# Kernel tuning notes

Measured on AMD Instinct MI355X. Metric: run time of the kernel, lower is better.

The kernel has to match this reference:

```python
import jax, jax.numpy as jnp
import numpy as np

VOCAB = 32000
D_MODEL = 768
D_STATE = 16
D_CONV = 4
EXPAND = 2
D_INNER = EXPAND * D_MODEL          # 1536
DT_RANK = (D_MODEL + 15) // 16      # 48
B, L = 2, 1024


def setup_inputs() -> dict:
    key = jax.random.key(0)
    ks = jax.random.split(key, 10)
    s = 0.02
    return {
        "input_ids": jax.random.randint(ks[0], (B, L), 0, VOCAB),
        "embedding": jax.random.normal(ks[1], (VOCAB, D_MODEL), jnp.float32) * s,
        "in_proj_w": jax.random.normal(ks[2], (D_MODEL, 2 * D_INNER), jnp.float32) * s,
        "conv_w": jax.random.normal(ks[3], (D_INNER, D_CONV), jnp.float32) * s,
        "conv_b": jnp.zeros((D_INNER,), jnp.float32),
        "x_proj_w": jax.random.normal(ks[4], (D_INNER, DT_RANK + 2 * D_STATE), jnp.float32) * s,
        "dt_proj_w": jax.random.normal(ks[5], (DT_RANK, D_INNER), jnp.float32) * s,
        "dt_proj_b": jax.random.normal(ks[6], (D_INNER,), jnp.float32) * 0.1,
        "A_log": jnp.log(jnp.broadcast_to(
            jnp.arange(1, D_STATE + 1, dtype=jnp.float32), (D_INNER, D_STATE))),
        "D": jnp.ones((D_INNER,), jnp.float32),
        "out_proj_w": jax.random.normal(ks[7], (D_INNER, D_MODEL), jnp.float32) * s,
        "lm_head_w": jax.random.normal(ks[8], (D_MODEL, VOCAB), jnp.float32) * s,
        "lm_head_b": jnp.zeros((VOCAB,), jnp.float32),
    }


def _mamba(x, in_proj_w, conv_w, conv_b, x_proj_w, dt_proj_w, dt_proj_b,
           A_log, D, out_proj_w):
    Bsz = x.shape[0]
    # input projection -> (x, z) gate branches, each [B,L,D_INNER]
    xz = x @ in_proj_w
    xi, z = jnp.split(xz, 2, axis=-1)
    # causal depthwise conv1d over time
    xc = jax.lax.conv_general_dilated(
        xi.transpose(0, 2, 1), conv_w[:, None, :],
        window_strides=(1,), padding=[(D_CONV - 1, 0)],
        feature_group_count=D_INNER,
        dimension_numbers=("NCH", "OIH", "NCH"))
    xa = jax.nn.silu(xc + conv_b[None, :, None]).transpose(0, 2, 1)  # [B,L,Din]
    # input-dependent SSM params
    dbl = xa @ x_proj_w                                   # [B,L,dt_rank+2N]
    dt = dbl[..., :DT_RANK]
    Bm = dbl[..., DT_RANK:DT_RANK + D_STATE]              # [B,L,N]
    Cm = dbl[..., DT_RANK + D_STATE:]                     # [B,L,N]
    dt = jax.nn.softplus(dt @ dt_proj_w + dt_proj_b)      # [B,L,Din]
    A = -jnp.exp(A_log)                                   # [Din,N]
    dA = jnp.exp(dt[..., None] * A)                       # [B,L,Din,N]
    dBu = dt[..., None] * Bm[:, :, None, :] * xa[..., None]

    def step(h, ins):
        dA_t, dBu_t, C_t = ins
        h = dA_t * h + dBu_t                              # [B,Din,N]
        return h, jnp.einsum("bdn,bn->bd", h, C_t)

    h0 = jnp.zeros((Bsz, D_INNER, D_STATE), x.dtype)
    _, ys = jax.lax.scan(
        step, h0,
        (dA.transpose(1, 0, 2, 3), dBu.transpose(1, 0, 2, 3),
         Cm.transpose(1, 0, 2)))
    y = ys.transpose(1, 0, 2) + xa * D                    # skip connection
    y = y * jax.nn.silu(z)                                # gate
    return y @ out_proj_w


def reference(input_ids, embedding, in_proj_w, conv_w, conv_b, x_proj_w,
              dt_proj_w, dt_proj_b, A_log, D, out_proj_w, lm_head_w, lm_head_b):
    x = embedding[input_ids]                              # [B,L,d_model]
    y = _mamba(x, in_proj_w, conv_w, conv_b, x_proj_w, dt_proj_w, dt_proj_b,
               A_log, D, out_proj_w)
    return y @ lm_head_w + lm_head_b                      # [B,L,vocab]
```

## Files before the change

kernel.cpp:

```cpp
#include <hip/hip_runtime.h>
#include <hip/hip_bf16.h>
#include <cstdio>
#include <cstdint>

#define B_SZ    2
#define L_SEQ   1024
#define DMODEL  768
#define DINNER  1536
#define DSTATE  16
#define DTRANK  48
#define VOCAB   32000
#define BL      (B_SZ * L_SEQ)
#define NCH     64
#define CLEN    16

typedef __bf16 bf16;
typedef __bf16 bf16x8 __attribute__((ext_vector_type(8)));
typedef __bf16 bf16x4 __attribute__((ext_vector_type(4)));
typedef float  f32x4  __attribute__((ext_vector_type(4)));

__device__ __forceinline__ void gload16(const void* g, void* l) {
  __builtin_amdgcn_global_load_lds(
      (const __attribute__((address_space(1))) void*)g,
      (__attribute__((address_space(3))) void*)l, 16, 0, 0);
}
__device__ __forceinline__ void memfence() { asm volatile("" ::: "memory"); }

__global__ void k_embed(const int* __restrict__ ids, const float* __restrict__ emb,
                        bf16* __restrict__ xh, bf16* __restrict__ xl) {
  const int row = blockIdx.x;
  const int id  = ids[row];
  const float4* s = (const float4*)(emb + (size_t)id * DMODEL);
  const int i = threadIdx.x;
  const float4 v = s[i];
  bf16x4 hv, lv;
  hv[0] = (bf16)v.x; hv[1] = (bf16)v.y; hv[2] = (bf16)v.z; hv[3] = (bf16)v.w;
  lv[0] = (bf16)(v.x - (float)hv[0]); lv[1] = (bf16)(v.y - (float)hv[1]);
  lv[2] = (bf16)(v.z - (float)hv[2]); lv[3] = (bf16)(v.w - (float)hv[3]);
  *(bf16x4*)(xh + (size_t)row * DMODEL + i * 4) = hv;
  *(bf16x4*)(xl + (size_t)row * DMODEL + i * 4) = lv;
}

template<bool SPLIT>
__global__ void k_tconv(const float* __restrict__ W, bf16* __restrict__ Th,
                        bf16* __restrict__ Tl, int K, int N) {
  __shared__ float t[32][33];
  const int n0 = blockIdx.x * 32;
  const int k0 = blockIdx.y * 32;
  const int tx = threadIdx.x;
  const int ty = threadIdx.y;
#pragma unroll
  for (int i = 0; i < 4; i++)
    t[ty + i * 8][tx] = W[(size_t)(k0 + ty + i * 8) * N + n0 + tx];
  __syncthreads();
#pragma unroll
  for (int i = 0; i < 4; i++) {
    const float v = t[tx][ty + i * 8];
    const bf16 hv = (bf16)v;
    Th[(size_t)(n0 + ty + i * 8) * K + k0 + tx] = hv;
    if constexpr (SPLIT)
      Tl[(size_t)(n0 + ty + i * 8) * K + k0 + tx] = (bf16)(v - (float)hv);
  }
}

template<bool SPLIT, bool BIAS, bool BF16OUT>
__global__ __launch_bounds__(256) void k_gemm(
    const bf16* __restrict__ Ah, const bf16* __restrict__ Al,
    const bf16* __restrict__ Bh, const bf16* __restrict__ Bl,
    const float* __restrict__ bias, float* __restrict__ C,
    int M, int N, int K) {
  __shared__ bf16 sAh[2][128 * 32];
  __shared__ bf16 sBh[2][128 * 32];
  __shared__ bf16 sAl[SPLIT ? 2 : 1][SPLIT ? 128 * 32 : 8];
  __shared__ bf16 sBl[SPLIT ? 2 : 1][SPLIT ? 128 * 32 : 8];

  const int tid  = threadIdx.x;
  const int lane = tid & 63;
  const int wave = tid >> 6;
  const int bm = blockIdx.y * 128;
  const int bn = blockIdx.x * 128;

  const int srow = tid >> 2;
  const int schk = (tid & 3) * 8;

  const bf16* gA0 = Ah + (size_t)(bm + srow) * K + schk;
  const bf16* gA1 = gA0 + (size_t)64 * K;
  const bf16* gB0 = Bh + (size_t)(bn + srow) * K + schk;
  const bf16* gB1 = gB0 + (size_t)64 * K;
  const bf16 *gA0l = nullptr, *gA1l = nullptr, *gB0l = nullptr, *gB1l = nullptr;
  if constexpr (SPLIT) {
    gA0l = Al + (size_t)(bm + srow) * K + schk;  gA1l = gA0l + (size_t)64 * K;
    gB0l = Bl + (size_t)(bn + srow) * K + schk;  gB1l = gB0l + (size_t)64 * K;
  }

  const int wm = (wave >> 1) * 64;
  const int wn = (wave & 1) * 64;
  const int lr = lane & 15;
  const int kg = lane >> 4;

  f32x4 acc[4][4] = {};
  const int nt = K >> 5;

#define STG(t_, b_) do {                                                    \
    const size_t ko_ = (size_t)(t_) * 32;                                   \
    gload16(gA0 + ko_, &sAh[b_][tid * 8]);                                  \
    gload16(gA1 + ko_, &sAh[b_][2048 + tid * 8]);                           \
    gload16(gB0 + ko_, &sBh[b_][tid * 8]);                                  \
    gload16(gB1 + ko_, &sBh[b_][2048 + tid * 8]);                           \
    if constexpr (SPLIT) {                                                  \
      gload16(gA0l + ko_, &sAl[b_][tid * 8]);                               \
      gload16(gA1l + ko_, &sAl[b_][2048 + tid * 8]);                        \
      gload16(gB0l + ko_, &sBl[b_][tid * 8]);                               \
      gload16(gB1l + ko_, &sBl[b_][2048 + tid * 8]);                        \
    }                                                                       \
  } while (0)

  STG(0, 0);
  asm volatile("s_waitcnt vmcnt(0)" ::: "memory");
  __builtin_amdgcn_s_barrier();
  memfence();

  for (int t = 0; t < nt; ++t) {
    const int b = t & 1;
    if (t + 1 < nt) STG(t + 1, b ^ 1);

    bf16x8 af[4], bfv[4];
#pragma unroll
    for (int i = 0; i < 4; i++)
      af[i] = *(const bf16x8*)&sAh[b][(wm + i * 16 + lr) * 32 + kg * 8];
#pragma unroll
    for (int i = 0; i < 4; i++)
      bfv[i] = *(const bf16x8*)&sBh[b][(wn + i * 16 + lr) * 32 + kg * 8];

#pragma unroll
    for (int mi = 0; mi < 4; mi++)
#pragma unroll
      for (int ni = 0; ni < 4; ni++)
        acc[mi][ni] = __builtin_amdgcn_mfma_f32_16x16x32_bf16(
            af[mi], bfv[ni], acc[mi][ni], 0, 0, 0);

    if constexpr (SPLIT) {
      bf16x8 afl[4], bfl[4];
#pragma unroll
      for (int i = 0; i < 4; i++)
        afl[i] = *(const bf16x8*)&sAl[b][(wm + i * 16 + lr) * 32 + kg * 8];
#pragma unroll
      for (int i = 0; i < 4; i++)
        bfl[i] = *(const bf16x8*)&sBl[b][(wn + i * 16 + lr) * 32 + kg * 8];
#pragma unroll
      for (int mi = 0; mi < 4; mi++)
#pragma unroll
        for (int ni = 0; ni < 4; ni++) {
          acc[mi][ni] = __builtin_amdgcn_mfma_f32_16x16x32_bf16(
              afl[mi], bfv[ni], acc[mi][ni], 0, 0, 0);
          acc[mi][ni] = __builtin_amdgcn_mfma_f32_16x16x32_bf16(
              af[mi], bfl[ni], acc[mi][ni], 0, 0, 0);
        }
    }

    asm volatile("s_waitcnt vmcnt(0)" ::: "memory");
    __builtin_amdgcn_s_barrier();
    memfence();
  }
#undef STG

#pragma unroll
  for (int mi = 0; mi < 4; mi++) {
#pragma unroll
    for (int ni = 0; ni < 4; ni++) {
      const int col = bn + wn + ni * 16 + lr;
      float bv = 0.f;
      if constexpr (BIAS) bv = bias[col];
#pragma unroll
      for (int r = 0; r < 4; r++) {
        const int row = bm + wm + mi * 16 + kg * 4 + r;
        if constexpr (BF16OUT)
          ((bf16*)C)[(size_t)row * N + col] = (bf16)(acc[mi][ni][r] + bv);
        else
          C[(size_t)row * N + col] = acc[mi][ni][r] + bv;
      }
    }
  }
}

__global__ __launch_bounds__(512, 4) void k_gemm8(
    const bf16* __restrict__ A, const bf16* __restrict__ Bt,
    const float* __restrict__ bias, float* __restrict__ C,
    int M, int N, int K, int mblocks) {
  extern __shared__ bf16 lds[];

  const int orig = (blockIdx.x & 7) * ((int)gridDim.x >> 3) + (blockIdx.x >> 3);
  const int bm = (orig % mblocks) * 128;
  const int bn = (orig / mblocks) * 256;

  const int tid  = threadIdx.x;
  const int lane = tid & 63;
  const int wave = tid >> 6;
  const int wm   = wave >> 2;
  const int wn   = wave & 3;
  const int lr   = lane & 15;
  const int kg   = lane >> 4;
  const int sw   = (lr >> 1) & 3;

  const int srA = (wave << 4) + (lane >> 2);
  const int srB = (wave << 5) + (lane >> 2);
  const int ssA = (lane & 3) ^ ((srA >> 1) & 3);
  const int ssB = (lane & 3) ^ ((srB >> 1) & 3);
  const size_t gAoff  = (size_t)(bm + srA) * K + ssA * 8;
  const size_t gBoff0 = (size_t)(bn + srB) * K + ssB * 8;
  const size_t gBoff1 = gBoff0 + (size_t)16 * K;

  const int aoff = (wm * 64 + lr) * 32 + ((kg ^ sw) << 3);
  const int boff = (wn * 64 + lr) * 32 + ((kg ^ sw) << 3);

  const int nt = K >> 5;

#define STAGE(ts_) do {                                                    \
    bf16* lb_ = lds + ((ts_) & 1) * 12288;                                 \
    const size_t ko_ = (size_t)(ts_) * 32;                                 \
    gload16(A  + gAoff  + ko_, lb_ + wave * 512);                          \
    gload16(Bt + gBoff0 + ko_, lb_ + 4096 + wave * 1024);                  \
    gload16(Bt + gBoff1 + ko_, lb_ + 4096 + wave * 1024 + 512);            \
  } while (0)

  f32x4 acc[4][4] = {};

  STAGE(0);
  asm volatile("s_waitcnt vmcnt(0)" ::: "memory");
  __builtin_amdgcn_s_barrier();
  memfence();

  for (int t = 0; t < nt; ++t) {
    if (t + 1 < nt) STAGE(t + 1);

    const bf16* lA = lds + (t & 1) * 12288;
    const bf16* lB = lA + 4096;

    bf16x8 bfr[4], afr[4];
#pragma unroll
    for (int j = 0; j < 4; j++) bfr[j] = *(const bf16x8*)(lB + boff + j * 512);
#pragma unroll
    for (int i = 0; i < 4; i++) afr[i] = *(const bf16x8*)(lA + aoff + i * 512);

    __builtin_amdgcn_s_setprio(1);
#pragma unroll
    for (int i = 0; i < 4; i++)
#pragma unroll
      for (int j = 0; j < 4; j++)
        acc[i][j] = __builtin_amdgcn_mfma_f32_16x16x32_bf16(afr[i], bfr[j], acc[i][j], 0, 0, 0);
    __builtin_amdgcn_s_setprio(0);

    asm volatile("s_waitcnt vmcnt(0)" ::: "memory");
    __builtin_amdgcn_s_barrier();
    memfence();
  }
#undef STAGE

  float bv[4];
#pragma unroll
  for (int j = 0; j < 4; j++)
    bv[j] = bias ? bias[bn + wn * 64 + j * 16 + lr] : 0.f;
#pragma unroll
  for (int i = 0; i < 4; i++) {
    const int row = bm + wm * 64 + i * 16 + kg * 4;
#pragma unroll
    for (int j = 0; j < 4; j++) {
      const int col = bn + wn * 64 + j * 16 + lr;
#pragma unroll
      for (int r = 0; r < 4; r++)
        C[(size_t)(row + r) * N + col] = acc[i][j][r] + bv[j];
    }
  }
}

__global__ void k_conv(const float* __restrict__ xz, const float* __restrict__ cw,
                       const float* __restrict__ cb, float* __restrict__ xa) {
  const int bl = blockIdx.x;
  const int l  = bl & (L_SEQ - 1);
  for (int d = threadIdx.x; d < DINNER; d += blockDim.x) {
    float acc = cb[d];
#pragma unroll
    for (int k = 0; k < 4; k++) {
      const int ll = l + k - 3;
      if (ll >= 0)
        acc = fmaf(xz[(size_t)(bl + k - 3) * (2 * DINNER) + d], cw[d * 4 + k], acc);
    }
    xa[(size_t)bl * DINNER + d] = acc / (1.f + __expf(-acc));
  }
}

__global__ void k_xproj(const float* __restrict__ xa, const float* __restrict__ w,
                        float* __restrict__ dbl) {
  const int t = threadIdx.x;
  const int r = blockIdx.x * 8 + t / 80;
  const int c = t % 80;
  const float* xr = xa + (size_t)r * DINNER;
  float acc = 0.f;
  for (int k = 0; k < DINNER; k++) acc = fmaf(xr[k], w[k * 80 + c], acc);
  dbl[(size_t)r * 80 + c] = acc;
}

__global__ __launch_bounds__(256) void k_dtproj(
    const float* __restrict__ dbl, const float* __restrict__ w,
    const float* __restrict__ bvec, float* __restrict__ dt) {
  const int r0 = blockIdx.x * 8;
  const int tid = threadIdx.x;
  __shared__ float ds[8][DTRANK];
  for (int i = tid; i < 8 * DTRANK; i += 256)
    ds[i / DTRANK][i % DTRANK] = dbl[(size_t)(r0 + i / DTRANK) * 80 + i % DTRANK];
  __syncthreads();
  for (int c = tid; c < DINNER; c += 256) {
    const float bvc = bvec[c];
    float acc[8];
#pragma unroll
    for (int j = 0; j < 8; j++) acc[j] = bvc;
    for (int k = 0; k < DTRANK; k++) {
      const float wv = w[(size_t)k * DINNER + c];
#pragma unroll
      for (int j = 0; j < 8; j++) acc[j] = fmaf(ds[j][k], wv, acc[j]);
    }
#pragma unroll
    for (int j = 0; j < 8; j++) {
      const float a = acc[j];
      dt[(size_t)(r0 + j) * DINNER + c] = (a > 20.f) ? a : log1pf(expf(a));
    }
  }
}

__global__ __launch_bounds__(256) void k_scan1(
    const float* __restrict__ dt, const float* __restrict__ dbl,
    const float* __restrict__ xa, const float* __restrict__ a_log,
    float* __restrict__ P, float* __restrict__ S) {
  const int tid = threadIdx.x;
  const int d = blockIdx.x * 256 + tid;
  const int c = blockIdx.y;
  const int b = blockIdx.z;
  __shared__ float sB[CLEN][DSTATE];
  {
    const int j = tid >> 4, n = tid & 15;
    sB[j][n] = dbl[(size_t)(b * L_SEQ + c * CLEN + j) * 80 + DTRANK + n];
  }
  __syncthreads();
  float a[16];
#pragma unroll
  for (int q = 0; q < 4; q++) {
    const float4 v = *(const float4*)&a_log[d * DSTATE + q * 4];
    a[q*4+0] = -expf(v.x); a[q*4+1] = -expf(v.y);
    a[q*4+2] = -expf(v.z); a[q*4+3] = -expf(v.w);
  }
  float h[16] = {}, p[16];
#pragma unroll
  for (int n = 0; n < 16; n++) p[n] = 1.f;
  const size_t rowb = (size_t)(b * L_SEQ + c * CLEN);
#pragma unroll 4
  for (int j = 0; j < CLEN; j++) {
    const size_t row = rowb + j;
    const float dtv = dt[row * DINNER + d];
    const float xav = xa[row * DINNER + d];
    const float du  = dtv * xav;
#pragma unroll
    for (int n = 0; n < 16; n++) {
      const float dA = __expf(dtv * a[n]);
      h[n] = fmaf(dA, h[n], du * sB[j][n]);
      p[n] *= dA;
    }
  }
  const size_t base = (((size_t)c * B_SZ + b) * DINNER + d) * DSTATE;
#pragma unroll
  for (int q = 0; q < 4; q++) {
    *(float4*)&P[base + q * 4] = make_float4(p[q*4], p[q*4+1], p[q*4+2], p[q*4+3]);
    *(float4*)&S[base + q * 4] = make_float4(h[q*4], h[q*4+1], h[q*4+2], h[q*4+3]);
  }
}

__global__ __launch_bounds__(256) void k_scan2(
    const float* __restrict__ P, const float* __restrict__ S,
    float* __restrict__ Hin) {
  const int gid = blockIdx.x * 256 + threadIdx.x;
  const int STRIDE = B_SZ * DINNER * DSTATE;
  float h = 0.f;
#pragma unroll 4
  for (int c = 0; c < NCH; c++) {
    Hin[(size_t)c * STRIDE + gid] = h;
    h = fmaf(P[(size_t)c * STRIDE + gid], h, S[(size_t)c * STRIDE + gid]);
  }
}

__global__ __launch_bounds__(256) void k_scan3(
    const float* __restrict__ dt, const float* __restrict__ dbl,
    const float* __restrict__ xa, const float* __restrict__ a_log,
    const float* __restrict__ dvec, const float* __restrict__ xz,
    const float* __restrict__ Hin, bf16* __restrict__ ych,
    bf16* __restrict__ ycl) {
  const int tid = threadIdx.x;
  const int d = blockIdx.x * 256 + tid;
  const int c = blockIdx.y;
  const int b = blockIdx.z;
  __shared__ float sB[CLEN][DSTATE];
  __shared__ float sC[CLEN][DSTATE];
  {
    const int j = tid >> 4, n = tid & 15;
    const size_t r80 = (size_t)(b * L_SEQ + c * CLEN + j) * 80;
    sB[j][n] = dbl[r80 + DTRANK + n];
    sC[j][n] = dbl[r80 + DTRANK + DSTATE + n];
  }
  __syncthreads();
  float a[16];
#pragma unroll
  for (int q = 0; q < 4; q++) {
    const float4 v = *(const float4*)&a_log[d * DSTATE + q * 4];
    a[q*4+0] = -expf(v.x); a[q*4+1] = -expf(v.y);
    a[q*4+2] = -expf(v.z); a[q*4+3] = -expf(v.w);
  }
  float h[16];
  const size_t base = (((size_t)c * B_SZ + b) * DINNER + d) * DSTATE;
#pragma unroll
  for (int q = 0; q < 4; q++) {
    const float4 v = *(const float4*)&Hin[base + q * 4];
    h[q*4+0] = v.x; h[q*4+1] = v.y; h[q*4+2] = v.z; h[q*4+3] = v.w;
  }
  const float Dv = dvec[d];
  const size_t rowb = (size_t)(b * L_SEQ + c * CLEN);
#pragma unroll 4
  for (int j = 0; j < CLEN; j++) {
    const size_t row = rowb + j;
    const float dtv = dt[row * DINNER + d];
    const float xav = xa[row * DINNER + d];
    const float du  = dtv * xav;
    float y = 0.f;
#pragma unroll
    for (int n = 0; n < 16; n++) {
      const float dA = __expf(dtv * a[n]);
      h[n] = fmaf(dA, h[n], du * sB[j][n]);
      y = fmaf(h[n], sC[j][n], y);
    }
    const float z  = xz[row * (2 * DINNER) + DINNER + d];
    const float sz = z / (1.f + __expf(-z));
    const float val = fmaf(xav, Dv, y) * sz;
    const bf16 hv = (bf16)val;
    ych[row * DINNER + d] = hv;
    ycl[row * DINNER + d] = (bf16)(val - (float)hv);
  }
}

extern "C" void kernel_launch(void* const* d_in, const int* in_sizes, int n_in,
                              void* d_out, int out_size, void* d_ws, size_t ws_size,
                              hipStream_t stream) {
  const int*   ids   = (const int*)d_in[0];
  const float* emb   = (const float*)d_in[1];
  const float* w_in  = (const float*)d_in[2];
  const float* cw    = (const float*)d_in[3];
  const float* cb    = (const float*)d_in[4];
  const float* w_x   = (const float*)d_in[5];
  const float* w_dt  = (const float*)d_in[6];
  const float* b_dt  = (const float*)d_in[7];
  const float* a_log = (const float*)d_in[8];
  const float* dvec  = (const float*)d_in[9];
  const float* w_out = (const float*)d_in[10];
  const float* w_lm  = (const float*)d_in[11];
  const float* b_lm  = (const float*)d_in[12];
  float* out = (float*)d_out;

  char* ws = (char*)d_ws;
  size_t off = 0;
  auto alloc = [&](size_t bytes) {
    void* p = ws + off;
    off = (off + bytes + 255) & ~(size_t)255;
    return p;
  };
  float* xw    = (float*)alloc((size_t)BL * DMODEL * 4);
  float* xz    = (float*)alloc((size_t)BL * 2 * DINNER * 4);
  float* xa    = (float*)alloc((size_t)BL * DINNER * 4);
  float* dbl   = (float*)alloc((size_t)BL * 80 * 4);
  float* dt    = (float*)alloc((size_t)BL * DINNER * 4);
  float* ycmb  = (float*)alloc((size_t)BL * DINNER * 4);
  float* yo    = (float*)alloc((size_t)BL * DMODEL * 4);
  bf16* xwh    = (bf16*)alloc((size_t)BL * DMODEL * 2);
  bf16* xwl    = (bf16*)alloc((size_t)BL * DMODEL * 2);
  bf16* wtinh  = (bf16*)alloc((size_t)3072 * DMODEL * 2);
  bf16* wtinl  = (bf16*)alloc((size_t)3072 * DMODEL * 2);
  bf16* ych    = (bf16*)alloc((size_t)BL * DINNER * 2);
  bf16* ycl    = (bf16*)alloc((size_t)BL * DINNER * 2);
  bf16* wtoh   = (bf16*)alloc((size_t)DMODEL * DINNER * 2);
  bf16* wtol   = (bf16*)alloc((size_t)DMODEL * DINNER * 2);
  bf16* yob    = (bf16*)alloc((size_t)BL * DMODEL * 2);
  bf16* wtlm   = (bf16*)alloc((size_t)VOCAB * DMODEL * 2);
  (void)xw; (void)ycmb; (void)yo;
  if (off > ws_size) {
    fprintf(stderr, "kernel_launch: ws too small (need %zu, have %zu)\n", off, ws_size);
    return;
  }

  float* Pbuf = (float*)xwh;
  float* Sbuf = (float*)ych;
  float* Hin  = (float*)wtlm;

  (void)hipFuncSetAttribute((const void*)k_gemm8,
                            hipFuncAttributeMaxDynamicSharedMemorySize, 65536);

  k_embed<<<BL, DMODEL / 4, 0, stream>>>(ids, emb, xwh, xwl);
  k_tconv<true><<<dim3(3072 / 32, DMODEL / 32), dim3(32, 8), 0, stream>>>(w_in, wtinh, wtinl, DMODEL, 3072);
  k_gemm<true, false, false><<<dim3(3072 / 128, BL / 128), 256, 0, stream>>>(
      xwh, xwl, wtinh, wtinl, nullptr, xz, BL, 3072, DMODEL);
  k_conv<<<BL, 256, 0, stream>>>(xz, cw, cb, xa);
  k_xproj<<<BL / 8, 640, 0, stream>>>(xa, w_x, dbl);
  k_dtproj<<<BL / 8, 256, 0, stream>>>(dbl, w_dt, b_dt, dt);
  k_scan1<<<dim3(DINNER / 256, NCH, B_SZ), 256, 0, stream>>>(dt, dbl, xa, a_log, Pbuf, Sbuf);
  k_scan2<<<(B_SZ * DINNER * DSTATE) / 256, 256, 0, stream>>>(Pbuf, Sbuf, Hin);
  k_scan3<<<dim3(DINNER / 256, NCH, B_SZ), 256, 0, stream>>>(dt, dbl, xa, a_log, dvec, xz, Hin, ych, ycl);
  k_tconv<true><<<dim3(DMODEL / 32, DINNER / 32), dim3(32, 8), 0, stream>>>(w_out, wtoh, wtol, DINNER, DMODEL);
  k_gemm<true, false, true><<<dim3(DMODEL / 128, BL / 128), 256, 0, stream>>>(
      ych, ycl, wtoh, wtol, nullptr, (float*)yob, BL, DMODEL, DINNER);
  k_tconv<false><<<dim3(VOCAB / 32, DMODEL / 32), dim3(32, 8), 0, stream>>>(w_lm, wtlm, nullptr, DMODEL, VOCAB);
  {
    const int mb = BL / 128;
    const int nb = VOCAB / 256;
    k_gemm8<<<mb * nb, 512, 49152, stream>>>(yob, wtlm, b_lm, out,
                                             BL, VOCAB, DMODEL, mb);
  }
}
```

Before: 467.4 us.

## Load GEMM A operand directly from global into registers, bypass LDS

Both GEMM kernels stop staging the A tile through shared memory. Each wave now loads its A fragments straight from global memory into registers at the top of every k-step, and only B stays double-buffered in LDS. The lm_head GEMM's dynamic LDS allocation shrinks to match, and B staging is re-indexed. This cuts LDS traffic and footprint, which may raise occupancy. The cost is that A global loads are issued per wave with no prefetch, so their latency sits directly before the MFMAs. A is also re-read by waves sharing the same rows, relying on cache.

```diff
diff --git a/kernel.cpp b/kernel.cpp
--- a/kernel.cpp
+++ b/kernel.cpp
@@ -69,9 +69,7 @@
     const bf16* __restrict__ Bh, const bf16* __restrict__ Bl,
     const float* __restrict__ bias, float* __restrict__ C,
     int M, int N, int K) {
-  __shared__ bf16 sAh[2][128 * 32];
   __shared__ bf16 sBh[2][128 * 32];
-  __shared__ bf16 sAl[SPLIT ? 2 : 1][SPLIT ? 128 * 32 : 8];
   __shared__ bf16 sBl[SPLIT ? 2 : 1][SPLIT ? 128 * 32 : 8];
 
   const int tid  = threadIdx.x;
@@ -83,13 +81,10 @@
   const int srow = tid >> 2;
   const int schk = (tid & 3) * 8;
 
-  const bf16* gA0 = Ah + (size_t)(bm + srow) * K + schk;
-  const bf16* gA1 = gA0 + (size_t)64 * K;
   const bf16* gB0 = Bh + (size_t)(bn + srow) * K + schk;
   const bf16* gB1 = gB0 + (size_t)64 * K;
-  const bf16 *gA0l = nullptr, *gA1l = nullptr, *gB0l = nullptr, *gB1l = nullptr;
+  const bf16 *gB0l = nullptr, *gB1l = nullptr;
   if constexpr (SPLIT) {
-    gA0l = Al + (size_t)(bm + srow) * K + schk;  gA1l = gA0l + (size_t)64 * K;
     gB0l = Bl + (size_t)(bn + srow) * K + schk;  gB1l = gB0l + (size_t)64 * K;
   }
 
@@ -98,18 +93,23 @@
   const int lr = lane & 15;
   const int kg = lane >> 4;
 
+  const bf16* gAh[4];
+  const bf16* gAl[4];
+#pragma unroll
+  for (int mi = 0; mi < 4; mi++) {
+    gAh[mi] = Ah + (size_t)(bm + wm + mi * 16 + lr) * K + kg * 8;
+    if constexpr (SPLIT)
+      gAl[mi] = Al + (size_t)(bm + wm + mi * 16 + lr) * K + kg * 8;
+  }
+
   f32x4 acc[4][4] = {};
   const int nt = K >> 5;
 
 #define STG(t_, b_) do {                                                    \
     const size_t ko_ = (size_t)(t_) * 32;                                   \
-    gload16(gA0 + ko_, &sAh[b_][tid * 8]);                                  \
-    gload16(gA1 + ko_, &sAh[b_][2048 + tid * 8]);                           \
     gload16(gB0 + ko_, &sBh[b_][tid * 8]);                                  \
     gload16(gB1 + ko_, &sBh[b_][2048 + tid * 8]);                           \
     if constexpr (SPLIT) {                                                  \
-      gload16(gA0l + ko_, &sAl[b_][tid * 8]);                               \
-      gload16(gA1l + ko_, &sAl[b_][2048 + tid * 8]);                        \
       gload16(gB0l + ko_, &sBl[b_][tid * 8]);                               \
       gload16(gB1l + ko_, &sBl[b_][2048 + tid * 8]);                        \
     }                                                                       \
@@ -122,12 +122,15 @@
 
   for (int t = 0; t < nt; ++t) {
     const int b = t & 1;
+    const int ko = t * 32;
+
+    bf16x8 af[4];
+#pragma unroll
+    for (int i = 0; i < 4; i++) af[i] = *(const bf16x8*)(gAh[i] + ko);
+
     if (t + 1 < nt) STG(t + 1, b ^ 1);
 
-    bf16x8 af[4], bfv[4];
-#pragma unroll
-    for (int i = 0; i < 4; i++)
-      af[i] = *(const bf16x8*)&sAh[b][(wm + i * 16 + lr) * 32 + kg * 8];
+    bf16x8 bfv[4];
 #pragma unroll
     for (int i = 0; i < 4; i++)
       bfv[i] = *(const bf16x8*)&sBh[b][(wn + i * 16 + lr) * 32 + kg * 8];
@@ -142,8 +145,7 @@
     if constexpr (SPLIT) {
       bf16x8 afl[4], bfl[4];
 #pragma unroll
-      for (int i = 0; i < 4; i++)
-        afl[i] = *(const bf16x8*)&sAl[b][(wm + i * 16 + lr) * 32 + kg * 8];
+      for (int i = 0; i < 4; i++) afl[i] = *(const bf16x8*)(gAl[i] + ko);
 #pragma unroll
       for (int i = 0; i < 4; i++)
         bfl[i] = *(const bf16x8*)&sBl[b][(wn + i * 16 + lr) * 32 + kg * 8];
@@ -202,45 +204,47 @@
   const int kg   = lane >> 4;
   const int sw   = (lr >> 1) & 3;
 
-  const int srA = (wave << 4) + (lane >> 2);
-  const int srB = (wave << 5) + (lane >> 2);
-  const int ssA = (lane & 3) ^ ((srA >> 1) & 3);
+  const int srB = (wave << 4) + (lane >> 2);
   const int ssB = (lane & 3) ^ ((srB >> 1) & 3);
-  const size_t gAoff  = (size_t)(bm + srA) * K + ssA * 8;
   const size_t gBoff0 = (size_t)(bn + srB) * K + ssB * 8;
-  const size_t gBoff1 = gBoff0 + (size_t)16 * K;
-
-  const int aoff = (wm * 64 + lr) * 32 + ((kg ^ sw) << 3);
+  const size_t gBoff1 = gBoff0 + (size_t)128 * K;
+
+  const bf16* gA[4];
+#pragma unroll
+  for (int i = 0; i < 4; i++)
+    gA[i] = A + (size_t)(bm + wm * 64 + i * 16 + lr) * K + kg * 8;
+
   const int boff = (wn * 64 + lr) * 32 + ((kg ^ sw) << 3);
 
   const int nt = K >> 5;
 
-#define STAGE(ts_) do {                                                    \
-    bf16* lb_ = lds + ((ts_) & 1) * 12288;                                 \
+#define STAGE_B(ts_) do {                                                  \
+    bf16* lb_ = lds + ((ts_) & 1) * 8192;                                  \
     const size_t ko_ = (size_t)(ts_) * 32;                                 \
-    gload16(A  + gAoff  + ko_, lb_ + wave * 512);                          \
-    gload16(Bt + gBoff0 + ko_, lb_ + 4096 + wave * 1024);                  \
-    gload16(Bt + gBoff1 + ko_, lb_ + 4096 + wave * 1024 + 512);            \
+    gload16(Bt + gBoff0 + ko_, lb_ + tid * 8);                             \
+    gload16(Bt + gBoff1 + ko_, lb_ + 4096 + tid * 8);                      \
   } while (0)
 
   f32x4 acc[4][4] = {};
 
-  STAGE(0);
+  STAGE_B(0);
   asm volatile("s_waitcnt vmcnt(0)" ::: "memory");
   __builtin_amdgcn_s_barrier();
   memfence();
 
   for (int t = 0; t < nt; ++t) {
-    if (t + 1 < nt) STAGE(t + 1);
-
-    const bf16* lA = lds + (t & 1) * 12288;
-    const bf16* lB = lA + 4096;
-
-    bf16x8 bfr[4], afr[4];
+    const int ko = t * 32;
+
+    bf16x8 afr[4];
+#pragma unroll
+    for (int i = 0; i < 4; i++) afr[i] = *(const bf16x8*)(gA[i] + ko);
+
+    if (t + 1 < nt) STAGE_B(t + 1);
+
+    const bf16* lB = lds + (t & 1) * 8192;
+    bf16x8 bfr[4];
 #pragma unroll
     for (int j = 0; j < 4; j++) bfr[j] = *(const bf16x8*)(lB + boff + j * 512);
-#pragma unroll
-    for (int i = 0; i < 4; i++) afr[i] = *(const bf16x8*)(lA + aoff + i * 512);
 
     __builtin_amdgcn_s_setprio(1);
 #pragma unroll
@@ -254,7 +258,7 @@
     __builtin_amdgcn_s_barrier();
     memfence();
   }
-#undef STAGE
+#undef STAGE_B
 
   float bv[4];
 #pragma unroll
@@ -515,7 +519,7 @@
   {
     const int mb = BL / 128;
     const int nb = VOCAB / 256;
-    k_gemm8<<<mb * nb, 512, 49152, stream>>>(yob, wtlm, b_lm, out,
+    k_gemm8<<<mb * nb, 512, 32768, stream>>>(yob, wtlm, b_lm, out,
                                              BL, VOCAB, DMODEL, mb);
   }
 }
```

New measurement: 607.2 us. +29.9%, slower.

## Pre-pack LM-head operands into MFMA fragment layout and load directly from global

Applied to the files above, without the earlier changes.

Replaces the LDS-staged 128x256 LM-head GEMM with a 128x128 kernel that reads operands straight from global memory into registers. The weight transpose now writes B in MFMA fragment order, and a new pack kernel rearranges A the same way, so each lane does one contiguous 16-byte load per fragment. This removes LDS traffic and barriers in the main loop, with register double-buffering across k-steps. In exchange it adds an extra pack kernel, loses LDS sharing of tiles between waves (more global/L2 traffic), and relies on cache hits for reuse.

```diff
diff --git a/kernel.cpp b/kernel.cpp
--- a/kernel.cpp
+++ b/kernel.cpp
@@ -13,6 +13,7 @@
 #define BL      (B_SZ * L_SEQ)
 #define NCH     64
 #define CLEN    16
+#define NKT     (DMODEL / 32)
 
 typedef __bf16 bf16;
 typedef __bf16 bf16x8 __attribute__((ext_vector_type(8)));
@@ -63,6 +64,37 @@
   }
 }
 
+__global__ void k_tconvp(const float* __restrict__ W, bf16* __restrict__ Bp,
+                         int K, int N) {
+  __shared__ float t[32][33];
+  const int n0 = blockIdx.x * 32;
+  const int k0 = blockIdx.y * 32;
+  const int tx = threadIdx.x;
+  const int ty = threadIdx.y;
+#pragma unroll
+  for (int i = 0; i < 4; i++)
+    t[ty + i * 8][tx] = W[(size_t)(k0 + ty + i * 8) * N + n0 + tx];
+  __syncthreads();
+  const int kt = k0 >> 5;
+#pragma unroll
+  for (int i = 0; i < 4; i++) {
+    const int n = n0 + ty + i * 8;
+    const int k = k0 + tx;
+    const float v = t[tx][ty + i * 8];
+    const int l = (((k & 31) >> 3) << 4) | (n & 15);
+    Bp[((size_t)(n >> 4) * NKT + kt) * 512 + l * 8 + (k & 7)] = (bf16)v;
+  }
+}
+
+__global__ void k_apack(const bf16* __restrict__ A, bf16* __restrict__ Ap) {
+  const int mt = blockIdx.x;
+  const int kt = blockIdx.y;
+  const int l  = threadIdx.x;
+  const int lr = l & 15, kg = l >> 4;
+  const bf16x8 v = *(const bf16x8*)(A + (size_t)(mt * 16 + lr) * DMODEL + kt * 32 + kg * 8);
+  *(bf16x8*)(Ap + ((size_t)mt * NKT + kt) * 512 + l * 8) = v;
+}
+
 template<bool SPLIT, bool BIAS, bool BF16OUT>
 __global__ __launch_bounds__(256) void k_gemm(
     const bf16* __restrict__ Ah, const bf16* __restrict__ Al,
@@ -183,83 +215,64 @@
   }
 }
 
-__global__ __launch_bounds__(512, 4) void k_gemm8(
-    const bf16* __restrict__ A, const bf16* __restrict__ Bt,
+__global__ __launch_bounds__(256, 3) void k_gemmp(
+    const bf16* __restrict__ Ap, const bf16* __restrict__ Bp,
     const float* __restrict__ bias, float* __restrict__ C,
-    int M, int N, int K, int mblocks) {
-  extern __shared__ bf16 lds[];
-
+    int M, int N, int mblocks) {
   const int orig = (blockIdx.x & 7) * ((int)gridDim.x >> 3) + (blockIdx.x >> 3);
   const int bm = (orig % mblocks) * 128;
-  const int bn = (orig / mblocks) * 256;
-
-  const int tid  = threadIdx.x;
-  const int lane = tid & 63;
-  const int wave = tid >> 6;
-  const int wm   = wave >> 2;
-  const int wn   = wave & 3;
+  const int bn = (orig / mblocks) * 128;
+
+  const int lane = threadIdx.x & 63;
+  const int wave = threadIdx.x >> 6;
+  const int wm   = wave >> 1;
+  const int wn   = wave & 1;
   const int lr   = lane & 15;
   const int kg   = lane >> 4;
-  const int sw   = (lr >> 1) & 3;
-
-  const int srA = (wave << 4) + (lane >> 2);
-  const int srB = (wave << 5) + (lane >> 2);
-  const int ssA = (lane & 3) ^ ((srA >> 1) & 3);
-  const int ssB = (lane & 3) ^ ((srB >> 1) & 3);
-  const size_t gAoff  = (size_t)(bm + srA) * K + ssA * 8;
-  const size_t gBoff0 = (size_t)(bn + srB) * K + ssB * 8;
-  const size_t gBoff1 = gBoff0 + (size_t)16 * K;
-
-  const int aoff = (wm * 64 + lr) * 32 + ((kg ^ sw) << 3);
-  const int boff = (wn * 64 + lr) * 32 + ((kg ^ sw) << 3);
-
-  const int nt = K >> 5;
-
-#define STAGE(ts_) do {                                                    \
-    bf16* lb_ = lds + ((ts_) & 1) * 12288;                                 \
-    const size_t ko_ = (size_t)(ts_) * 32;                                 \
-    gload16(A  + gAoff  + ko_, lb_ + wave * 512);                          \
-    gload16(Bt + gBoff0 + ko_, lb_ + 4096 + wave * 1024);                  \
-    gload16(Bt + gBoff1 + ko_, lb_ + 4096 + wave * 1024 + 512);            \
-  } while (0)
+
+  const bf16* pA = Ap + ((size_t)((bm >> 4) + wm * 4) * NKT) * 512 + lane * 8;
+  const bf16* pB = Bp + ((size_t)((bn >> 4) + wn * 4) * NKT) * 512 + lane * 8;
 
   f32x4 acc[4][4] = {};
-
-  STAGE(0);
-  asm volatile("s_waitcnt vmcnt(0)" ::: "memory");
-  __builtin_amdgcn_s_barrier();
-  memfence();
-
-  for (int t = 0; t < nt; ++t) {
-    if (t + 1 < nt) STAGE(t + 1);
-
-    const bf16* lA = lds + (t & 1) * 12288;
-    const bf16* lB = lA + 4096;
-
-    bf16x8 bfr[4], afr[4];
-#pragma unroll
-    for (int j = 0; j < 4; j++) bfr[j] = *(const bf16x8*)(lB + boff + j * 512);
-#pragma unroll
-    for (int i = 0; i < 4; i++) afr[i] = *(const bf16x8*)(lA + aoff + i * 512);
-
-    __builtin_amdgcn_s_setprio(1);
+  bf16x8 a0[4], b0[4], a1[4], b1[4];
+
+#pragma unroll
+  for (int i = 0; i < 4; i++) {
+    a0[i] = *(const bf16x8*)(pA + (size_t)i * NKT * 512);
+    b0[i] = *(const bf16x8*)(pB + (size_t)i * NKT * 512);
+  }
+
+#pragma unroll 1
+  for (int kt = 0; kt < NKT; kt += 2) {
+#pragma unroll
+    for (int i = 0; i < 4; i++) {
+      a1[i] = *(const bf16x8*)(pA + (size_t)i * NKT * 512 + (kt + 1) * 512);
+      b1[i] = *(const bf16x8*)(pB + (size_t)i * NKT * 512 + (kt + 1) * 512);
+    }
 #pragma unroll
     for (int i = 0; i < 4; i++)
 #pragma unroll
       for (int j = 0; j < 4; j++)
-        acc[i][j] = __builtin_amdgcn_mfma_f32_16x16x32_bf16(afr[i], bfr[j], acc[i][j], 0, 0, 0);
-    __builtin_amdgcn_s_setprio(0);
-
-    asm volatile("s_waitcnt vmcnt(0)" ::: "memory");
-    __builtin_amdgcn_s_barrier();
-    memfence();
-  }
-#undef STAGE
+        acc[i][j] = __builtin_amdgcn_mfma_f32_16x16x32_bf16(a0[i], b0[j], acc[i][j], 0, 0, 0);
+
+    if (kt + 2 < NKT) {
+#pragma unroll
+      for (int i = 0; i < 4; i++) {
+        a0[i] = *(const bf16x8*)(pA + (size_t)i * NKT * 512 + (kt + 2) * 512);
+        b0[i] = *(const bf16x8*)(pB + (size_t)i * NKT * 512 + (kt + 2) * 512);
+      }
+    }
+#pragma unroll
+    for (int i = 0; i < 4; i++)
+#pragma unroll
+      for (int j = 0; j < 4; j++)
+        acc[i][j] = __builtin_amdgcn_mfma_f32_16x16x32_bf16(a1[i], b1[j], acc[i][j], 0, 0, 0);
+  }
 
   float bv[4];
 #pragma unroll
   for (int j = 0; j < 4; j++)
-    bv[j] = bias ? bias[bn + wn * 64 + j * 16 + lr] : 0.f;
+    bv[j] = bias[bn + wn * 64 + j * 16 + lr];
 #pragma unroll
   for (int i = 0; i < 4; i++) {
     const int row = bm + wm * 64 + i * 16 + kg * 4;
@@ -485,7 +498,7 @@
   bf16* wtol   = (bf16*)alloc((size_t)DMODEL * DINNER * 2);
   bf16* yob    = (bf16*)alloc((size_t)BL * DMODEL * 2);
   bf16* wtlm   = (bf16*)alloc((size_t)VOCAB * DMODEL * 2);
-  (void)xw; (void)ycmb; (void)yo;
+  (void)ycmb; (void)yo;
   if (off > ws_size) {
     fprintf(stderr, "kernel_launch: ws too small (need %zu, have %zu)\n", off, ws_size);
     return;
@@ -494,9 +507,8 @@
   float* Pbuf = (float*)xwh;
   float* Sbuf = (float*)ych;
   float* Hin  = (float*)wtlm;
-
-  (void)hipFuncSetAttribute((const void*)k_gemm8,
-                            hipFuncAttributeMaxDynamicSharedMemorySize, 65536);
+  bf16*  Bp   = wtlm;
+  bf16*  Ap   = (bf16*)xw;
 
   k_embed<<<BL, DMODEL / 4, 0, stream>>>(ids, emb, xwh, xwl);
   k_tconv<true><<<dim3(3072 / 32, DMODEL / 32), dim3(32, 8), 0, stream>>>(w_in, wtinh, wtinl, DMODEL, 3072);
@@ -511,11 +523,11 @@
   k_tconv<true><<<dim3(DMODEL / 32, DINNER / 32), dim3(32, 8), 0, stream>>>(w_out, wtoh, wtol, DINNER, DMODEL);
   k_gemm<true, false, true><<<dim3(DMODEL / 128, BL / 128), 256, 0, stream>>>(
       ych, ycl, wtoh, wtol, nullptr, (float*)yob, BL, DMODEL, DINNER);
-  k_tconv<false><<<dim3(VOCAB / 32, DMODEL / 32), dim3(32, 8), 0, stream>>>(w_lm, wtlm, nullptr, DMODEL, VOCAB);
+  k_tconvp<<<dim3(VOCAB / 32, DMODEL / 32), dim3(32, 8), 0, stream>>>(w_lm, Bp, DMODEL, VOCAB);
+  k_apack<<<dim3(BL / 16, NKT), 64, 0, stream>>>(yob, Ap);
   {
     const int mb = BL / 128;
-    const int nb = VOCAB / 256;
-    k_gemm8<<<mb * nb, 512, 49152, stream>>>(yob, wtlm, b_lm, out,
-                                             BL, VOCAB, DMODEL, mb);
-  }
-}
+    const int nb = VOCAB / 128;
+    k_gemmp<<<mb * nb, 256, 0, stream>>>(Ap, Bp, b_lm, out, BL, VOCAB, mb);
+  }
+}
```

New measurement: 482.0 us. +3.1%, slower.

## Enlarge LM-head GEMM tile to 256x256 with 4 waves each computing 128x128

Applied to the files above, without the earlier changes.

The LM-head GEMM moves from 128x256 tiles with 8 waves (64x64 per wave) to 256x256 tiles with 4 waves, each accumulating a 128x128 sub-tile with 64 MFMA accumulators. Each LDS fragment is reused across more MFMAs and global traffic per output drops, while the grid halves to 1000 blocks. The cost is a large accumulator register footprint (256 VGPR/AGPR for acc alone) plus launch bounds that allow one block, which limits occupancy and latency hiding and may cause spills. Bias is now read without a null check.

```diff
diff --git a/kernel.cpp b/kernel.cpp
--- a/kernel.cpp
+++ b/kernel.cpp
@@ -183,47 +183,49 @@
   }
 }
 
-__global__ __launch_bounds__(512, 4) void k_gemm8(
+__global__ __launch_bounds__(256, 1) void k_gemmw(
     const bf16* __restrict__ A, const bf16* __restrict__ Bt,
     const float* __restrict__ bias, float* __restrict__ C,
     int M, int N, int K, int mblocks) {
   extern __shared__ bf16 lds[];
 
   const int orig = (blockIdx.x & 7) * ((int)gridDim.x >> 3) + (blockIdx.x >> 3);
-  const int bm = (orig % mblocks) * 128;
+  const int bm = (orig % mblocks) * 256;
   const int bn = (orig / mblocks) * 256;
 
   const int tid  = threadIdx.x;
   const int lane = tid & 63;
   const int wave = tid >> 6;
-  const int wm   = wave >> 2;
-  const int wn   = wave & 3;
+  const int wm   = wave >> 1;
+  const int wn   = wave & 1;
   const int lr   = lane & 15;
   const int kg   = lane >> 4;
   const int sw   = (lr >> 1) & 3;
 
-  const int srA = (wave << 4) + (lane >> 2);
-  const int srB = (wave << 5) + (lane >> 2);
-  const int ssA = (lane & 3) ^ ((srA >> 1) & 3);
-  const int ssB = (lane & 3) ^ ((srB >> 1) & 3);
-  const size_t gAoff  = (size_t)(bm + srA) * K + ssA * 8;
-  const size_t gBoff0 = (size_t)(bn + srB) * K + ssB * 8;
-  const size_t gBoff1 = gBoff0 + (size_t)16 * K;
-
-  const int aoff = (wm * 64 + lr) * 32 + ((kg ^ sw) << 3);
-  const int boff = (wn * 64 + lr) * 32 + ((kg ^ sw) << 3);
+  const int srow  = tid >> 2;
+  const int sslot = (tid & 3) ^ ((srow >> 1) & 3);
+  const size_t gA = (size_t)(bm + srow) * K + sslot * 8;
+  const size_t gB = (size_t)(bn + srow) * K + sslot * 8;
+
+  const int aoff = (wm * 128 + lr) * 32 + ((kg ^ sw) << 3);
+  const int boff = (wn * 128 + lr) * 32 + ((kg ^ sw) << 3);
 
   const int nt = K >> 5;
 
 #define STAGE(ts_) do {                                                    \
-    bf16* lb_ = lds + ((ts_) & 1) * 12288;                                 \
+    bf16* lb_ = lds + ((ts_) & 1) * 16384;                                 \
     const size_t ko_ = (size_t)(ts_) * 32;                                 \
-    gload16(A  + gAoff  + ko_, lb_ + wave * 512);                          \
-    gload16(Bt + gBoff0 + ko_, lb_ + 4096 + wave * 1024);                  \
-    gload16(Bt + gBoff1 + ko_, lb_ + 4096 + wave * 1024 + 512);            \
+    gload16(A  + gA + ko_,                  lb_ + tid * 8);                \
+    gload16(A  + gA +  64 * (size_t)K + ko_, lb_ + 2048 + tid * 8);        \
+    gload16(A  + gA + 128 * (size_t)K + ko_, lb_ + 4096 + tid * 8);        \
+    gload16(A  + gA + 192 * (size_t)K + ko_, lb_ + 6144 + tid * 8);        \
+    gload16(Bt + gB + ko_,                  lb_ + 8192 + tid * 8);         \
+    gload16(Bt + gB +  64 * (size_t)K + ko_, lb_ + 10240 + tid * 8);       \
+    gload16(Bt + gB + 128 * (size_t)K + ko_, lb_ + 12288 + tid * 8);       \
+    gload16(Bt + gB + 192 * (size_t)K + ko_, lb_ + 14336 + tid * 8);       \
   } while (0)
 
-  f32x4 acc[4][4] = {};
+  f32x4 acc[8][8] = {};
 
   STAGE(0);
   asm volatile("s_waitcnt vmcnt(0)" ::: "memory");
@@ -233,20 +235,20 @@
   for (int t = 0; t < nt; ++t) {
     if (t + 1 < nt) STAGE(t + 1);
 
-    const bf16* lA = lds + (t & 1) * 12288;
-    const bf16* lB = lA + 4096;
-
-    bf16x8 bfr[4], afr[4];
-#pragma unroll
-    for (int j = 0; j < 4; j++) bfr[j] = *(const bf16x8*)(lB + boff + j * 512);
-#pragma unroll
-    for (int i = 0; i < 4; i++) afr[i] = *(const bf16x8*)(lA + aoff + i * 512);
+    const bf16* lA = lds + (t & 1) * 16384;
+    const bf16* lB = lA + 8192;
+
+    bf16x8 bfr[8], afr[8];
+#pragma unroll
+    for (int j = 0; j < 8; j++) bfr[j] = *(const bf16x8*)(lB + boff + j * 512);
+#pragma unroll
+    for (int i = 0; i < 8; i++) afr[i] = *(const bf16x8*)(lA + aoff + i * 512);
 
     __builtin_amdgcn_s_setprio(1);
 #pragma unroll
-    for (int i = 0; i < 4; i++)
-#pragma unroll
-      for (int j = 0; j < 4; j++)
+    for (int i = 0; i < 8; i++)
+#pragma unroll
+      for (int j = 0; j < 8; j++)
         acc[i][j] = __builtin_amdgcn_mfma_f32_16x16x32_bf16(afr[i], bfr[j], acc[i][j], 0, 0, 0);
     __builtin_amdgcn_s_setprio(0);
 
@@ -256,16 +258,16 @@
   }
 #undef STAGE
 
-  float bv[4];
-#pragma unroll
-  for (int j = 0; j < 4; j++)
-    bv[j] = bias ? bias[bn + wn * 64 + j * 16 + lr] : 0.f;
-#pragma unroll
-  for (int i = 0; i < 4; i++) {
-    const int row = bm + wm * 64 + i * 16 + kg * 4;
-#pragma unroll
-    for (int j = 0; j < 4; j++) {
-      const int col = bn + wn * 64 + j * 16 + lr;
+  float bv[8];
+#pragma unroll
+  for (int j = 0; j < 8; j++)
+    bv[j] = bias[bn + wn * 128 + j * 16 + lr];
+#pragma unroll
+  for (int i = 0; i < 8; i++) {
+    const int row = bm + wm * 128 + i * 16 + kg * 4;
+#pragma unroll
+    for (int j = 0; j < 8; j++) {
+      const int col = bn + wn * 128 + j * 16 + lr;
 #pragma unroll
       for (int r = 0; r < 4; r++)
         C[(size_t)(row + r) * N + col] = acc[i][j][r] + bv[j];
@@ -495,7 +497,7 @@
   float* Sbuf = (float*)ych;
   float* Hin  = (float*)wtlm;
 
-  (void)hipFuncSetAttribute((const void*)k_gemm8,
+  (void)hipFuncSetAttribute((const void*)k_gemmw,
                             hipFuncAttributeMaxDynamicSharedMemorySize, 65536);
 
   k_embed<<<BL, DMODEL / 4, 0, stream>>>(ids, emb, xwh, xwl);
@@ -513,9 +515,9 @@
       ych, ycl, wtoh, wtol, nullptr, (float*)yob, BL, DMODEL, DINNER);
   k_tconv<false><<<dim3(VOCAB / 32, DMODEL / 32), dim3(32, 8), 0, stream>>>(w_lm, wtlm, nullptr, DMODEL, VOCAB);
   {
-    const int mb = BL / 128;
+    const int mb = BL / 256;
     const int nb = VOCAB / 256;
-    k_gemm8<<<mb * nb, 512, 49152, stream>>>(yob, wtlm, b_lm, out,
+    k_gemmw<<<mb * nb, 256, 65536, stream>>>(yob, wtlm, b_lm, out,
                                              BL, VOCAB, DMODEL, mb);
   }
 }
```

Result: no change. 466.4 us (-0.2%).
